# Kernel optimization log

Measured on AMD Instinct MI355X. Metric: run time of the kernel, lower is better.

## Reference

```python
import jax, jax.numpy as jnp
import numpy as np

B, N, C = 8, 1024, 1024
H = 16
D = C // H  # head_dim = 64


def apply_rope(t, cos, sin):
    # t: (B,H,N,D), cos/sin: (N, D//2). Interleaved-pair RoPE
    # (matches repeat_interleave(2) + stack(-y2,y1) in the torch code).
    tr = t.reshape(*t.shape[:-1], D // 2, 2)
    t1, t2 = tr[..., 0], tr[..., 1]
    o1 = t1 * cos - t2 * sin
    o2 = t2 * cos + t1 * sin
    return jnp.stack((o1, o2), axis=-1).reshape(t.shape)


def setup_inputs() -> dict:
    key = jax.random.key(0)
    k1, k2, k3, k4 = jax.random.split(key, 4)
    s = 0.02
    x = jax.random.normal(k1, (B, N, C), dtype=jnp.float32)
    w_qkv = jax.random.normal(k2, (C, 3 * C), dtype=jnp.float32) * s  # qkv_bias=False
    w_proj = jax.random.normal(k3, (C, C), dtype=jnp.float32) * s
    b_proj = jax.random.normal(k4, (C,), dtype=jnp.float32) * s
    return {"x": x, "w_qkv": w_qkv, "w_proj": w_proj, "b_proj": b_proj}


def reference(x, w_qkv, w_proj, b_proj):
    # QKV projection: (B,N,3C) -> (3,B,H,N,D)
    qkv = (x @ w_qkv).reshape(B, N, 3, H, D).transpose(2, 0, 3, 1, 4)
    q, k, v = qkv[0], qkv[1], qkv[2]

    # RoPE tables: pos = arange(N) (mask=None, no cls/registers)
    pos = jnp.arange(N, dtype=jnp.float32)
    omega = 1.0 / (10000.0 ** (jnp.arange(D // 2, dtype=jnp.float32) / (D / 2.0)))
    freq = pos[:, None] * omega  # (N, D//2)
    cos, sin = jnp.cos(freq), jnp.sin(freq)

    q = apply_rope(q, cos, sin)
    k = apply_rope(k, cos, sin)

    # Scaled dot-product attention (non-causal, no dropout in eval)
    scale = 1.0 / jnp.sqrt(jnp.float32(D))
    scores = jnp.einsum('bhqd,bhkd->bhqk', q, k) * scale
    attn = jax.nn.softmax(scores, axis=-1)
    out = jnp.einsum('bhqk,bhkd->bhqd', attn, v)

    # Merge heads + output projection
    out = out.transpose(0, 2, 1, 3).reshape(B, N, C)
    return out @ w_proj + b_proj
```

## Files before the change

### kernel.cpp

```cpp
#include <hip/hip_runtime.h>
#include <hip/hip_bf16.h>
#include <math.h>

#define Bsz  8
#define Nseq 1024
#define Cdim 1024
#define Hh   16
#define Dd   64

typedef short short8 __attribute__((ext_vector_type(8)));
typedef float floatx4 __attribute__((ext_vector_type(4)));

__device__ __forceinline__ unsigned short f2bf(float f) {
    __hip_bfloat16 h = __float2bfloat16(f);
    return __builtin_bit_cast(unsigned short, h);
}
__device__ __forceinline__ float b2f(unsigned short u) {
    return __uint_as_float(((unsigned)u) << 16);
}

__device__ __forceinline__ void async16(const void* g, void* l) {
    __builtin_amdgcn_global_load_lds(
        (const __attribute__((address_space(1))) unsigned int*)g,
        (__attribute__((address_space(3))) unsigned int*)l, 16, 0, 0);
}

__device__ __forceinline__ unsigned pack_bf16(float lo, float hi) {
    unsigned ulo = __float_as_uint(lo) + 0x8000u;
    unsigned uhi = __float_as_uint(hi) + 0x8000u;
    return __builtin_amdgcn_perm(uhi, ulo, 0x07060302);
}

__global__ __launch_bounds__(256) void prep(
    const float* __restrict__ x, const float* __restrict__ w_qkv,
    const float* __restrict__ w_proj,
    unsigned short* __restrict__ xb, unsigned short* __restrict__ wqkvt,
    unsigned short* __restrict__ wprojt, float2* __restrict__ rope)
{
    __shared__ float T[64][65];
    const int blk = blockIdx.x;
    const int tid = threadIdx.x;

    if (blk < 8192) {
        int i = blk * 256 + tid;
        float4 v = ((const float4*)x)[i];
        ushort4 u;
        u.x = f2bf(v.x); u.y = f2bf(v.y); u.z = f2bf(v.z); u.w = f2bf(v.w);
        ((ushort4*)xb)[i] = u;
        return;
    }
    if (blk < 9216) {
        const float* in;
        unsigned short* out;
        int R = 1024, Ccols, c0, r0;
        if (blk < 8960) {
            int b2 = blk - 8192;
            in = w_qkv; out = wqkvt; Ccols = 3072;
            c0 = (b2 % 48) * 64; r0 = (b2 / 48) * 64;
        } else {
            int b2 = blk - 8960;
            in = w_proj; out = wprojt; Ccols = 1024;
            c0 = (b2 % 16) * 64; r0 = (b2 / 16) * 64;
        }
        for (int i = tid; i < 4096; i += 256) {
            int r = i >> 6, c = i & 63;
            T[r][c] = in[(size_t)(r0 + r) * Ccols + c0 + c];
        }
        __syncthreads();
        for (int i = tid; i < 4096; i += 256) {
            int rr = i >> 6, cc = i & 63;
            out[(size_t)(c0 + rr) * R + r0 + cc] = f2bf(T[cc][rr]);
        }
        return;
    }
    {
        int i = (blk - 9216) * 256 + tid;
        int n = i >> 5, p = i & 31;
        float omega = __expf(-(float)p * 0.2878231366242557f);
        float sv, cv;
        sincosf((float)n * omega, &sv, &cv);
        rope[i] = make_float2(cv, sv);
    }
}

__global__ __launch_bounds__(256) void scatter(
    const unsigned short* __restrict__ qkv, const float2* __restrict__ rope,
    unsigned short* __restrict__ qb, unsigned short* __restrict__ kb,
    unsigned short* __restrict__ vt)
{
    __shared__ unsigned short T[64][68];
    const int blk = blockIdx.x;
    const int tid = threadIdx.x;

    if (blk < 16384) {
        int i = blk * 256 + tid;
        int row = i >> 9;
        int col = (i & 511) * 4;
        int sec = col >> 10;
        int cc  = col & 1023;
        int h = cc >> 6, d = cc & 63;
        int b = row >> 10, n = row & 1023;

        ushort4 v = *(const ushort4*)(qkv + (size_t)row * 3072 + sec * 1024 + cc);
        float2 cs0 = rope[n * 32 + (d >> 1)];
        float2 cs1 = rope[n * 32 + (d >> 1) + 1];
        float x0 = b2f(v.x), x1 = b2f(v.y), x2 = b2f(v.z), x3 = b2f(v.w);
        float scale = (sec == 0) ? 0.125f : 1.f;
        ushort4 o;
        o.x = f2bf((x0 * cs0.x - x1 * cs0.y) * scale);
        o.y = f2bf((x1 * cs0.x + x0 * cs0.y) * scale);
        o.z = f2bf((x2 * cs1.x - x3 * cs1.y) * scale);
        o.w = f2bf((x3 * cs1.x + x2 * cs1.y) * scale);
        unsigned short* dst = (sec == 0) ? qb : kb;
        *(ushort4*)(dst + (((size_t)(b * Hh + h) * Nseq + n) * Dd + d)) = o;
        return;
    }
    {
        int b2 = blk - 16384;
        int nt = b2 & 15, bh = b2 >> 4;
        int b = bh >> 4, h = bh & 15;
        for (int i = tid; i < 1024; i += 256) {
            int r = i >> 4, c4 = i & 15;
            const unsigned short* src =
                qkv + (size_t)(b * 1024 + nt * 64 + r) * 3072 + 2048 + h * 64;
            ushort4 v = ((const ushort4*)src)[c4];
            T[c4 * 4 + 0][r] = v.x;
            T[c4 * 4 + 1][r] = v.y;
            T[c4 * 4 + 2][r] = v.z;
            T[c4 * 4 + 3][r] = v.w;
        }
        __syncthreads();
        const size_t obase = (size_t)bh * Dd * Nseq + (size_t)nt * 64;
        for (int i = tid; i < 1024; i += 256) {
            int d = i >> 4, seg = i & 15;
            ushort4 v = *(const ushort4*)&T[d][seg * 4];
            *(ushort4*)(vt + obase + (size_t)d * Nseq + seg * 4) = v;
        }
    }
}

template <int MODE>
__global__ __launch_bounds__(256) void gemm_bf16(
    const unsigned short* __restrict__ A, const unsigned short* __restrict__ Bt,
    const float* __restrict__ bias,
    unsigned short* __restrict__ qkv, float* __restrict__ out)
{
    const int K = 1024;
    const int NW = (MODE == 0) ? 3072 : 1024;
    __shared__ short As[128][32];
    __shared__ short Bs[128][32];
    const int tid  = threadIdx.x;
    const int wave = tid >> 6, lane = tid & 63;
    const int ml = lane & 15, quad = lane >> 4;
    const int wm = wave >> 1, wn = wave & 1;
    const int bm = blockIdx.y * 128, bn = blockIdx.x * 128;

    const int gchunk = ((lane & 3) ^ ((lane >> 3) & 3)) * 8;
    const int srow   = lane >> 2;
    const int rslot  = (quad ^ ((ml >> 1) & 3)) * 8;

    floatx4 acc[4][4] = {};

    for (int k0 = 0; k0 < K; k0 += 32) {
        #pragma unroll
        for (int t = 0; t < 2; ++t) {
            int r0  = wave * 16 + t * 64;
            int row = r0 + srow;
            int kp  = k0 + gchunk;
            async16(A  + (size_t)(bm + row) * K + kp, &As[r0][0]);
            async16(Bt + (size_t)(bn + row) * K + kp, &Bs[r0][0]);
        }
        __syncthreads();

        short8 araw[4], braw[4];
        #pragma unroll
        for (int mi = 0; mi < 4; ++mi)
            araw[mi] = *(const short8*)&As[wm * 64 + mi * 16 + ml][rslot];
        #pragma unroll
        for (int ni = 0; ni < 4; ++ni)
            braw[ni] = *(const short8*)&Bs[wn * 64 + ni * 16 + ml][rslot];
        #pragma unroll
        for (int mi = 0; mi < 4; ++mi)
            #pragma unroll
            for (int ni = 0; ni < 4; ++ni)
                acc[mi][ni] = __builtin_amdgcn_mfma_f32_16x16x32_bf16(
                    araw[mi], braw[ni], acc[mi][ni], 0, 0, 0);
        __syncthreads();
    }

    if (MODE == 0) {
        #pragma unroll
        for (int ni = 0; ni < 4; ++ni) {
            int col = bn + wn * 64 + ni * 16 + ml;
            #pragma unroll
            for (int mi = 0; mi < 4; ++mi)
                #pragma unroll
                for (int r = 0; r < 4; ++r) {
                    int row = bm + wm * 64 + mi * 16 + quad * 4 + r;
                    qkv[(size_t)row * NW + col] = f2bf(acc[mi][ni][r]);
                }
        }
    } else {
        #pragma unroll
        for (int ni = 0; ni < 4; ++ni) {
            int col = bn + wn * 64 + ni * 16 + ml;
            float bv = bias[col];
            #pragma unroll
            for (int mi = 0; mi < 4; ++mi)
                #pragma unroll
                for (int r = 0; r < 4; ++r) {
                    int row = bm + wm * 64 + mi * 16 + quad * 4 + r;
                    out[(size_t)row * NW + col] = acc[mi][ni][r] + bv;
                }
        }
    }
}

__global__ __launch_bounds__(256) void attn_flash_mfma(
    const unsigned short* __restrict__ qb, const unsigned short* __restrict__ kb,
    const unsigned short* __restrict__ vt, unsigned short* __restrict__ ao)
{
    const int bh  = blockIdx.x;
    const int qt  = blockIdx.y;
    const int tid = threadIdx.x;
    const int wave = tid >> 6, lane = tid & 63;
    const int ml = lane & 15, quad = lane >> 4;
    const int lr = lane >> 3;
    const int lc = ((lane & 7) ^ lr) * 8;

    __shared__ short Qs[128][64];
    __shared__ short Ks[64][64];
    __shared__ short Vs[64][64];
    __shared__ short Ps[4][32][72];

    const size_t hbase = (size_t)bh * (Nseq * Dd);
    const size_t vbase = (size_t)bh * 64;
    const int q0 = qt * 128;
    const int wq = wave * 32;
    const int wk = wave * 16;

    #pragma unroll
    for (int t = 0; t < 4; ++t)
        async16(qb + hbase + (size_t)(q0 + wq + t * 8 + lr) * 64 + lc, &Qs[wq + t * 8][0]);
    async16(kb + hbase + (size_t)(wk + lr) * 64 + lc,     &Ks[wk][0]);
    async16(kb + hbase + (size_t)(wk + 8 + lr) * 64 + lc, &Ks[wk + 8][0]);
    __syncthreads();

    short8 qfr[2][2];
    #pragma unroll
    for (int ks = 0; ks < 2; ++ks) {
        const int sl = ((ks * 4 + quad) ^ (ml & 7)) * 8;
        qfr[ks][0] = *(const short8*)&Qs[wq + ml][sl];
        qfr[ks][1] = *(const short8*)&Qs[wq + 16 + ml][sl];
    }

    float l0 = 0.f, l1 = 0.f;
    floatx4 o[2][4] = {};

    for (int kt = 0; kt < 16; ++kt) {
        const int k0r = kt * 64;
        async16(vt + (vbase + wk + lr) * Nseq + k0r + lc,     &Vs[wk][0]);
        async16(vt + (vbase + wk + 8 + lr) * Nseq + k0r + lc, &Vs[wk + 8][0]);

        floatx4 st[2][4] = {};
        #pragma unroll
        for (int ks = 0; ks < 2; ++ks) {
            const int sl = ((ks * 4 + quad) ^ (ml & 7)) * 8;
            #pragma unroll
            for (int kbk = 0; kbk < 4; ++kbk) {
                short8 kf = *(const short8*)&Ks[kbk * 16 + ml][sl];
                st[0][kbk] = __builtin_amdgcn_mfma_f32_16x16x32_bf16(kf, qfr[ks][0], st[0][kbk], 0, 0, 0);
                st[1][kbk] = __builtin_amdgcn_mfma_f32_16x16x32_bf16(kf, qfr[ks][1], st[1][kbk], 0, 0, 0);
            }
        }

        #pragma unroll
        for (int qg = 0; qg < 2; ++qg) {
            float lacc = 0.f;
            #pragma unroll
            for (int kbk = 0; kbk < 4; ++kbk) {
                float e0 = __expf(st[qg][kbk][0]);
                float e1 = __expf(st[qg][kbk][1]);
                float e2 = __expf(st[qg][kbk][2]);
                float e3 = __expf(st[qg][kbk][3]);
                lacc += (e0 + e1) + (e2 + e3);
                uint2 pk;
                pk.x = pack_bf16(e0, e1);
                pk.y = pack_bf16(e2, e3);
                *(uint2*)&Ps[wave][qg * 16 + ml][kbk * 16 + quad * 4] = pk;
            }
            if (qg == 0) l0 += lacc; else l1 += lacc;
        }
        __syncthreads();

        if (kt < 15) {
            const int k1r = k0r + 64;
            async16(kb + hbase + (size_t)(k1r + wk + lr) * 64 + lc,     &Ks[wk][0]);
            async16(kb + hbase + (size_t)(k1r + wk + 8 + lr) * 64 + lc, &Ks[wk + 8][0]);
        }

        #pragma unroll
        for (int ks = 0; ks < 2; ++ks) {
            const int sl = ((ks * 4 + quad) ^ (ml & 7)) * 8;
            short8 pf0 = *(const short8*)&Ps[wave][ml][ks * 32 + quad * 8];
            short8 pf1 = *(const short8*)&Ps[wave][16 + ml][ks * 32 + quad * 8];
            #pragma unroll
            for (int nt = 0; nt < 4; ++nt) {
                short8 vf = *(const short8*)&Vs[nt * 16 + ml][sl];
                o[0][nt] = __builtin_amdgcn_mfma_f32_16x16x32_bf16(pf0, vf, o[0][nt], 0, 0, 0);
                o[1][nt] = __builtin_amdgcn_mfma_f32_16x16x32_bf16(pf1, vf, o[1][nt], 0, 0, 0);
            }
        }
        if (kt < 15)
            __syncthreads();
    }

    l0 += __shfl_xor(l0, 16);
    l0 += __shfl_xor(l0, 32);
    l1 += __shfl_xor(l1, 16);
    l1 += __shfl_xor(l1, 32);

    const int b = bh >> 4, h = bh & 15;
    #pragma unroll
    for (int qg = 0; qg < 2; ++qg) {
        float lsrc = (qg == 0) ? l0 : l1;
        #pragma unroll
        for (int r = 0; r < 4; ++r) {
            float lq = __shfl(lsrc, quad * 4 + r);
            float inv = 1.f / lq;
            int q = q0 + wq + qg * 16 + quad * 4 + r;
            size_t rowbase = ((size_t)(b * Nseq + q)) * Cdim + h * Dd;
            #pragma unroll
            for (int nt = 0; nt < 4; ++nt)
                ao[rowbase + nt * 16 + ml] = f2bf(o[qg][nt][r] * inv);
        }
    }
}

extern "C" void kernel_launch(void* const* d_in, const int* in_sizes, int n_in,
                              void* d_out, int out_size, void* d_ws, size_t ws_size,
                              hipStream_t stream) {
    const float* x      = (const float*)d_in[0];
    const float* w_qkv  = (const float*)d_in[1];
    const float* w_proj = (const float*)d_in[2];
    const float* b_proj = (const float*)d_in[3];
    float* out = (float*)d_out;

    const size_t M8 = (size_t)8 * 1024 * 1024;
    unsigned short* qb     = (unsigned short*)d_ws;
    unsigned short* kb     = qb + M8;
    unsigned short* vt     = kb + M8;
    unsigned short* xb     = vt + M8;
    unsigned short* wqkvt  = xb + M8;
    unsigned short* wprojt = wqkvt + 3 * 1024 * 1024;
    float2*         rope   = (float2*)(wprojt + 1024 * 1024);
    unsigned short* qkvws  = (unsigned short*)(rope + 32768);
    unsigned short* aob    = xb;

    prep<<<9344, 256, 0, stream>>>(x, w_qkv, w_proj, xb, wqkvt, wprojt, rope);

    gemm_bf16<0><<<dim3(24, 64), 256, 0, stream>>>(xb, wqkvt, nullptr, qkvws, nullptr);

    scatter<<<18432, 256, 0, stream>>>(qkvws, rope, qb, kb, vt);

    attn_flash_mfma<<<dim3(128, 8), 256, 0, stream>>>(qb, kb, vt, aob);

    gemm_bf16<1><<<dim3(8, 64), 256, 0, stream>>>(aob, wprojt, b_proj, nullptr, out);
}
```

Baseline: 255.2 us.

## Fuse RoPE and head scatter into QKV GEMM epilogue; widen K tile to 64

Removes the separate scatter kernel by applying RoPE, the Q scaling and the per-head layout writes directly in the QKV GEMM epilogue. The V block is transposed through shared memory there as well. The main loop now stages 64-wide K tiles with an XOR swizzle, halving the number of barriers per K sweep. This saves a full write and read of the intermediate qkv buffer and one kernel launch. In exchange the epilogue gains extra synchronisation, a lane shuffle for the RoPE pair partner, and scalar 2-byte scattered stores for Q and K.

```diff
diff --git a/kernel.cpp b/kernel.cpp
--- a/kernel.cpp
+++ b/kernel.cpp
@@ -83,134 +83,131 @@
     }
 }
 
-__global__ __launch_bounds__(256) void scatter(
-    const unsigned short* __restrict__ qkv, const float2* __restrict__ rope,
-    unsigned short* __restrict__ qb, unsigned short* __restrict__ kb,
-    unsigned short* __restrict__ vt)
-{
-    __shared__ unsigned short T[64][68];
-    const int blk = blockIdx.x;
-    const int tid = threadIdx.x;
-
-    if (blk < 16384) {
-        int i = blk * 256 + tid;
-        int row = i >> 9;
-        int col = (i & 511) * 4;
-        int sec = col >> 10;
-        int cc  = col & 1023;
-        int h = cc >> 6, d = cc & 63;
-        int b = row >> 10, n = row & 1023;
-
-        ushort4 v = *(const ushort4*)(qkv + (size_t)row * 3072 + sec * 1024 + cc);
-        float2 cs0 = rope[n * 32 + (d >> 1)];
-        float2 cs1 = rope[n * 32 + (d >> 1) + 1];
-        float x0 = b2f(v.x), x1 = b2f(v.y), x2 = b2f(v.z), x3 = b2f(v.w);
-        float scale = (sec == 0) ? 0.125f : 1.f;
-        ushort4 o;
-        o.x = f2bf((x0 * cs0.x - x1 * cs0.y) * scale);
-        o.y = f2bf((x1 * cs0.x + x0 * cs0.y) * scale);
-        o.z = f2bf((x2 * cs1.x - x3 * cs1.y) * scale);
-        o.w = f2bf((x3 * cs1.x + x2 * cs1.y) * scale);
-        unsigned short* dst = (sec == 0) ? qb : kb;
-        *(ushort4*)(dst + (((size_t)(b * Hh + h) * Nseq + n) * Dd + d)) = o;
-        return;
-    }
-    {
-        int b2 = blk - 16384;
-        int nt = b2 & 15, bh = b2 >> 4;
-        int b = bh >> 4, h = bh & 15;
-        for (int i = tid; i < 1024; i += 256) {
-            int r = i >> 4, c4 = i & 15;
-            const unsigned short* src =
-                qkv + (size_t)(b * 1024 + nt * 64 + r) * 3072 + 2048 + h * 64;
-            ushort4 v = ((const ushort4*)src)[c4];
-            T[c4 * 4 + 0][r] = v.x;
-            T[c4 * 4 + 1][r] = v.y;
-            T[c4 * 4 + 2][r] = v.z;
-            T[c4 * 4 + 3][r] = v.w;
-        }
-        __syncthreads();
-        const size_t obase = (size_t)bh * Dd * Nseq + (size_t)nt * 64;
-        for (int i = tid; i < 1024; i += 256) {
-            int d = i >> 4, seg = i & 15;
-            ushort4 v = *(const ushort4*)&T[d][seg * 4];
-            *(ushort4*)(vt + obase + (size_t)d * Nseq + seg * 4) = v;
-        }
-    }
-}
-
 template <int MODE>
 __global__ __launch_bounds__(256) void gemm_bf16(
     const unsigned short* __restrict__ A, const unsigned short* __restrict__ Bt,
-    const float* __restrict__ bias,
-    unsigned short* __restrict__ qkv, float* __restrict__ out)
+    const float* __restrict__ bias, const float2* __restrict__ rope,
+    unsigned short* __restrict__ qb, unsigned short* __restrict__ kb,
+    unsigned short* __restrict__ vtb, float* __restrict__ out)
 {
     const int K = 1024;
-    const int NW = (MODE == 0) ? 3072 : 1024;
-    __shared__ short As[128][32];
-    __shared__ short Bs[128][32];
+    __shared__ short SM[2][128][64];
     const int tid  = threadIdx.x;
     const int wave = tid >> 6, lane = tid & 63;
     const int ml = lane & 15, quad = lane >> 4;
     const int wm = wave >> 1, wn = wave & 1;
     const int bm = blockIdx.y * 128, bn = blockIdx.x * 128;
 
-    const int gchunk = ((lane & 3) ^ ((lane >> 3) & 3)) * 8;
-    const int srow   = lane >> 2;
-    const int rslot  = (quad ^ ((ml >> 1) & 3)) * 8;
+    const int lr     = lane >> 3;
+    const int lchunk = ((lane & 7) ^ lr) * 8;
 
     floatx4 acc[4][4] = {};
 
-    for (int k0 = 0; k0 < K; k0 += 32) {
-        #pragma unroll
-        for (int t = 0; t < 2; ++t) {
-            int r0  = wave * 16 + t * 64;
-            int row = r0 + srow;
-            int kp  = k0 + gchunk;
-            async16(A  + (size_t)(bm + row) * K + kp, &As[r0][0]);
-            async16(Bt + (size_t)(bn + row) * K + kp, &Bs[r0][0]);
+    for (int k0 = 0; k0 < K; k0 += 64) {
+        #pragma unroll
+        for (int t = 0; t < 4; ++t) {
+            int r8  = (wave * 4 + t) * 8;
+            int row = r8 + lr;
+            async16(A  + (size_t)(bm + row) * K + k0 + lchunk, &SM[0][r8][0]);
+            async16(Bt + (size_t)(bn + row) * K + k0 + lchunk, &SM[1][r8][0]);
         }
         __syncthreads();
 
-        short8 araw[4], braw[4];
-        #pragma unroll
-        for (int mi = 0; mi < 4; ++mi)
-            araw[mi] = *(const short8*)&As[wm * 64 + mi * 16 + ml][rslot];
-        #pragma unroll
-        for (int ni = 0; ni < 4; ++ni)
-            braw[ni] = *(const short8*)&Bs[wn * 64 + ni * 16 + ml][rslot];
-        #pragma unroll
-        for (int mi = 0; mi < 4; ++mi)
+        #pragma unroll
+        for (int ks = 0; ks < 2; ++ks) {
+            const int sl = ((ks * 4 + quad) ^ (ml & 7)) * 8;
+            short8 araw[4], braw[4];
+            #pragma unroll
+            for (int mi = 0; mi < 4; ++mi)
+                araw[mi] = *(const short8*)&SM[0][wm * 64 + mi * 16 + ml][sl];
             #pragma unroll
             for (int ni = 0; ni < 4; ++ni)
-                acc[mi][ni] = __builtin_amdgcn_mfma_f32_16x16x32_bf16(
-                    araw[mi], braw[ni], acc[mi][ni], 0, 0, 0);
+                braw[ni] = *(const short8*)&SM[1][wn * 64 + ni * 16 + ml][sl];
+            #pragma unroll
+            for (int mi = 0; mi < 4; ++mi)
+                #pragma unroll
+                for (int ni = 0; ni < 4; ++ni)
+                    acc[mi][ni] = __builtin_amdgcn_mfma_f32_16x16x32_bf16(
+                        araw[mi], braw[ni], acc[mi][ni], 0, 0, 0);
+        }
         __syncthreads();
     }
 
     if (MODE == 0) {
+        const int region = bn >> 10;
+        const int b = bm >> 10;
+        if (region < 2) {
+            float2* Rs = (float2*)&SM[0][0][0];
+            #pragma unroll
+            for (int t = 0; t < 16; ++t) {
+                int idx = t * 256 + tid;
+                Rs[idx] = rope[(size_t)((bm + (idx >> 5)) & 1023) * 32 + (idx & 31)];
+            }
+            __syncthreads();
+            unsigned short* dst = (region == 0) ? qb : kb;
+            const float scale = (region == 0) ? 0.125f : 1.f;
+            const float sgn = (ml & 1) ? 1.f : -1.f;
+            #pragma unroll
+            for (int ni = 0; ni < 4; ++ni) {
+                int col = bn + wn * 64 + ni * 16 + ml;
+                int jj = col & 1023;
+                int h = jj >> 6, d = jj & 63;
+                int p = d >> 1;
+                #pragma unroll
+                for (int mi = 0; mi < 4; ++mi)
+                    #pragma unroll
+                    for (int r = 0; r < 4; ++r) {
+                        int rl = wm * 64 + mi * 16 + quad * 4 + r;
+                        int n  = (bm + rl) & 1023;
+                        float val = acc[mi][ni][r];
+                        float partner = __shfl_xor(val, 1);
+                        float2 cs = Rs[rl * 32 + p];
+                        dst[(((size_t)(b * Hh + h)) * Nseq + n) * Dd + d] =
+                            f2bf((val * cs.x + sgn * partner * cs.y) * scale);
+                    }
+            }
+        } else {
+            short* T = &SM[0][0][0];
+            const int n0 = bm & 1023;
+            #pragma unroll
+            for (int hw = 0; hw < 2; ++hw) {
+                if (hw) __syncthreads();
+                if (wn == hw) {
+                    #pragma unroll
+                    for (int ni = 0; ni < 4; ++ni) {
+                        int dcol = ni * 16 + ml;
+                        #pragma unroll
+                        for (int mi = 0; mi < 4; ++mi)
+                            #pragma unroll
+                            for (int r = 0; r < 4; ++r) {
+                                int rl = wm * 64 + mi * 16 + quad * 4 + r;
+                                T[dcol * 132 + rl] = (short)f2bf(acc[mi][ni][r]);
+                            }
+                    }
+                }
+                __syncthreads();
+                int h = ((bn & 1023) >> 6) + hw;
+                #pragma unroll
+                for (int t = 0; t < 8; ++t) {
+                    int idx4 = t * 256 + tid;
+                    int d = idx4 >> 5, seg = idx4 & 31;
+                    ushort4 v4 = *(const ushort4*)&T[d * 132 + seg * 4];
+                    *(ushort4*)(vtb + (((size_t)(b * Hh + h)) * Dd + d) * Nseq
+                                + n0 + seg * 4) = v4;
+                }
+            }
+        }
+    } else {
         #pragma unroll
         for (int ni = 0; ni < 4; ++ni) {
             int col = bn + wn * 64 + ni * 16 + ml;
+            float bv = bias[col];
             #pragma unroll
             for (int mi = 0; mi < 4; ++mi)
                 #pragma unroll
                 for (int r = 0; r < 4; ++r) {
                     int row = bm + wm * 64 + mi * 16 + quad * 4 + r;
-                    qkv[(size_t)row * NW + col] = f2bf(acc[mi][ni][r]);
-                }
-        }
-    } else {
-        #pragma unroll
-        for (int ni = 0; ni < 4; ++ni) {
-            int col = bn + wn * 64 + ni * 16 + ml;
-            float bv = bias[col];
-            #pragma unroll
-            for (int mi = 0; mi < 4; ++mi)
-                #pragma unroll
-                for (int r = 0; r < 4; ++r) {
-                    int row = bm + wm * 64 + mi * 16 + quad * 4 + r;
-                    out[(size_t)row * NW + col] = acc[mi][ni][r] + bv;
+                    out[(size_t)row * 1024 + col] = acc[mi][ni][r] + bv;
                 }
         }
     }
@@ -354,16 +351,15 @@
     unsigned short* wqkvt  = xb + M8;
     unsigned short* wprojt = wqkvt + 3 * 1024 * 1024;
     float2*         rope   = (float2*)(wprojt + 1024 * 1024);
-    unsigned short* qkvws  = (unsigned short*)(rope + 32768);
     unsigned short* aob    = xb;
 
     prep<<<9344, 256, 0, stream>>>(x, w_qkv, w_proj, xb, wqkvt, wprojt, rope);
 
-    gemm_bf16<0><<<dim3(24, 64), 256, 0, stream>>>(xb, wqkvt, nullptr, qkvws, nullptr);
-
-    scatter<<<18432, 256, 0, stream>>>(qkvws, rope, qb, kb, vt);
+    gemm_bf16<0><<<dim3(24, 64), 256, 0, stream>>>(xb, wqkvt, nullptr, rope,
+                                                   qb, kb, vt, nullptr);
 
     attn_flash_mfma<<<dim3(128, 8), 256, 0, stream>>>(qb, kb, vt, aob);
 
-    gemm_bf16<1><<<dim3(8, 64), 256, 0, stream>>>(aob, wprojt, b_proj, nullptr, out);
-}
+    gemm_bf16<1><<<dim3(8, 64), 256, 0, stream>>>(aob, wprojt, b_proj, nullptr,
+                                                  nullptr, nullptr, nullptr, out);
+}
```

Result: faster. 246.1 us (-3.6%).
